# Optimization experiments

Hardware: AMD Instinct MI355X
Metric: run time of the kernel (lower is better)

## Reference

```python
import jax, jax.numpy as jnp
import numpy as np

B, NDEL, K, T = 32, 16, 10, 16384
N0 = int(round(T / 8))


def setup_inputs() -> dict:
    key = jax.random.key(0)
    k1, k2, k3 = jax.random.split(key, 3)
    shape = (B, NDEL, K)
    # stable complex-conjugate pole pairs: radius < 1 so the cascade decays
    r = jax.random.uniform(k1, shape, minval=0.5, maxval=0.99)
    theta = jax.random.uniform(k2, shape, minval=0.05, maxval=np.pi - 0.05)
    a1 = -2.0 * r * jnp.cos(theta)
    a2 = r * r
    b = jax.random.normal(k3, shape + (3,)) * 0.5
    # sos layout per biquad: (b0, b1, b2, a0, a1, a2), a0 = 1
    sos = jnp.concatenate(
        [b, jnp.ones(shape + (1,)), a1[..., None], a2[..., None]], axis=-1
    ).astype(jnp.float32)
    return {"output_biquad_cascade": sos}


def _sos_filter_impulse(sos):
    """Cascade-biquad IIR filter of a unit impulse.
    sos: [L, K, 6] -> output [L, T]. Transposed direct-form II, scan over time,
    vectorized over the L = B*Ndel independent filter lines."""
    L = sos.shape[0]
    a0 = sos[..., 3:4]
    bc = sos[..., 0:3] / a0  # [L, K, 3]
    ac = sos[..., 4:6] / a0  # [L, K, 2]
    # impulse input, time-major for scan: [T, L]
    x = jnp.zeros((T, L), dtype=sos.dtype).at[0, :].set(1.0)
    for k in range(K):  # fixed small cascade depth
        b0, b1, b2 = bc[:, k, 0], bc[:, k, 1], bc[:, k, 2]
        a1, a2 = ac[:, k, 0], ac[:, k, 1]

        def step(z, xt):
            z1, z2 = z
            y = b0 * xt + z1
            z1n = b1 * xt - a1 * y + z2
            z2n = b2 * xt - a2 * y
            return (z1n, z2n), y

        zero = jnp.zeros((L,), dtype=sos.dtype)
        _, x = jax.lax.scan(step, (zero, zero), x)  # x: [T, L]
    return x.T  # [L, T]


def reference(output_biquad_cascade):
    sos = output_biquad_cascade.reshape(B * NDEL, K, 6)
    y = _sos_filter_impulse(sos)  # [B*Ndel, T]
    # decay ratio: tail energy / head energy
    gamma = jnp.sum(jnp.abs(y[:, T - N0:]), axis=1) / jnp.sum(
        jnp.abs(y[:, :N0]), axis=1
    )
    gamma = gamma.reshape(B, NDEL)
    w = jnp.exp(gamma)
    loss = jnp.sum(gamma * w, axis=1) / jnp.sum(w, axis=1)  # softmax-weighted mean
    return jnp.sum(loss)
```

## Files before the change

### kernel.cpp

```cpp
#include <hip/hip_runtime.h>

#pragma clang fp contract(off)

#define B_    32
#define NDEL_ 16
#define K_    10
#define T_    16384
#define N0_   2048

__device__ __forceinline__ float dpp_shr1(float v) {
    int i = __builtin_bit_cast(int, v);
    int r = __builtin_amdgcn_update_dpp(0, i, 0x111 , 0xF, 0xF, true);
    return __builtin_bit_cast(float, r);
}

__global__ __launch_bounds__(256, 1)
void sos_gamma_kernel(const float* __restrict__ sos, float* __restrict__ out) {
#pragma clang fp contract(off)
    __builtin_amdgcn_s_setreg(6401, 0xC);

    const int tid  = threadIdx.x;
    const int wave = tid >> 6;
    const int lane = tid & 63;
    const int row  = lane >> 4;
    const int st   = lane & 15;
    const int d    = (wave << 2) | row;
    const int line = blockIdx.x * NDEL_ + d;

    float b0 = 0.f, b1 = 0.f, b2 = 0.f, a1 = 0.f, a2 = 0.f;
    if (st < K_) {
        const float* c = sos + (size_t)line * (K_ * 6) + st * 6;
        const float a0 = c[3];
        b0 = c[0] / a0;
        b1 = c[1] / a0;
        b2 = c[2] / a0;
        a1 = c[4] / a0;
        a2 = c[5] / a0;
    }

    float z1 = 0.f, z2 = 0.f;
    float hacc = 0.f, tacc = 0.f;

    float yA = 0.f, yB = 0.f;
    float xb1 = (st == 0) ? 1.0f : 0.0f;
    float xb2 = 0.f;

#define STEPX(XV, YOUT)                                \
    do {                                               \
        float x_ = (XV);                               \
        YOUT     = __builtin_fmaf(b0, x_, z1);         \
        float t3 = a1 * YOUT;                          \
        float t4 = __builtin_fmaf(b1, x_, -t3);        \
        float t6 = a2 * YOUT;                          \
        z1       = t4 + z2;                            \
        z2       = __builtin_fmaf(b2, x_, -t6);        \
    } while (0)

#define NOACC(YV)  do { } while (0)
#define HACC(YV)   do { hacc += fabsf(YV); } while (0)
#define TACC(YV)   do { tacc += fabsf(YV); } while (0)

#define TICK2(ACCUM)                                        \
    do {                                                    \
        float xA = xb1; xb2 = dpp_shr1(yA);                 \
        STEPX(xA, yB); ACCUM(yB);                           \
        float xB = xb2; xb1 = dpp_shr1(yB);                 \
        STEPX(xB, yA); ACCUM(yA);                           \
    } while (0)

#pragma unroll
    for (int p = 0; p < 9; ++p)    { TICK2(NOACC); }
#pragma unroll 4
    for (int p = 0; p < 1024; ++p) { TICK2(HACC); }
#pragma unroll 4
    for (int p = 0; p < 6144; ++p) { TICK2(NOACC); }
#pragma unroll 4
    for (int p = 0; p < 1024; ++p) { TICK2(TACC); }

#undef TICK2
#undef STEPX
#undef NOACC
#undef HACC
#undef TACC

    __shared__ float gam[NDEL_];
    if (st == 9) gam[d] = tacc / hacc;
    __syncthreads();

    if (tid == 0) {
        float num = 0.f, den = 0.f;
        for (int i = 0; i < NDEL_; ++i) {
            float g = gam[i];
            float w = expf(g);
            num += g * w;
            den += w;
        }
        atomicAdd(out, num / den);
    }
}

extern "C" void kernel_launch(void* const* d_in, const int* in_sizes, int n_in,
                              void* d_out, int out_size, void* d_ws, size_t ws_size,
                              hipStream_t stream) {
    (void)in_sizes; (void)n_in; (void)d_ws; (void)ws_size; (void)out_size;
    const float* sos = (const float*)d_in[0];
    float* out = (float*)d_out;

    hipMemsetAsync(out, 0, sizeof(float), stream);

    sos_gamma_kernel<<<B_, 256, 0, stream>>>(sos, out);
}
```

Baseline: 291.9 us.

## Split each batch across two blocks with a global atomic reduction

The grid doubles to 64 blocks. Each block handles 8 of the 16 delay lines of a batch, and each wave now runs only two filter lines (rows 0-1) instead of four. Per-line gamma values go to a workspace through atomics, and the second block to finish a batch does the softmax-weighted reduction. This spreads the work over more CUs, but adds an extra memset, global atomics and half-idle waves, while the serial recurrence length per lane stays the same.

Result: slower. 306.2 us (+4.9%).

```diff
diff --git a/kernel.cpp b/kernel.cpp
--- a/kernel.cpp
+++ b/kernel.cpp
@@ -15,7 +15,8 @@
 }
 
 __global__ __launch_bounds__(256, 1)
-void sos_gamma_kernel(const float* __restrict__ sos, float* __restrict__ out) {
+void sos_gamma_kernel(const float* __restrict__ sos, float* __restrict__ out,
+                      float* __restrict__ gws, int* __restrict__ cnt) {
 #pragma clang fp contract(off)
     __builtin_amdgcn_s_setreg(6401, 0xC);
 
@@ -24,26 +25,29 @@
     const int lane = tid & 63;
     const int row  = lane >> 4;
     const int st   = lane & 15;
-    const int d    = (wave << 2) | row;
-    const int line = blockIdx.x * NDEL_ + d;
+    const int g    = blockIdx.x;
+    const int b    = g >> 1;
+    const int d    = ((g & 1) << 3) | (wave << 1) | row;
+    const int line = b * NDEL_ + d;
 
-    float b0 = 0.f, b1 = 0.f, b2 = 0.f, a1 = 0.f, a2 = 0.f;
-    if (st < K_) {
-        const float* c = sos + (size_t)line * (K_ * 6) + st * 6;
-        const float a0 = c[3];
-        b0 = c[0] / a0;
-        b1 = c[1] / a0;
-        b2 = c[2] / a0;
-        a1 = c[4] / a0;
-        a2 = c[5] / a0;
-    }
+    if (row < 2) {
+        float b0 = 0.f, b1 = 0.f, b2 = 0.f, a1 = 0.f, a2 = 0.f;
+        if (st < K_) {
+            const float* c = sos + (size_t)line * (K_ * 6) + st * 6;
+            const float a0 = c[3];
+            b0 = c[0] / a0;
+            b1 = c[1] / a0;
+            b2 = c[2] / a0;
+            a1 = c[4] / a0;
+            a2 = c[5] / a0;
+        }
 
-    float z1 = 0.f, z2 = 0.f;
-    float hacc = 0.f, tacc = 0.f;
+        float z1 = 0.f, z2 = 0.f;
+        float hacc = 0.f, tacc = 0.f;
 
-    float yA = 0.f, yB = 0.f;
-    float xb1 = (st == 0) ? 1.0f : 0.0f;
-    float xb2 = 0.f;
+        float yA = 0.f, yB = 0.f;
+        float xb1 = (st == 0) ? 1.0f : 0.0f;
+        float xb2 = 0.f;
 
 #define STEPX(XV, YOUT)                                \
     do {                                               \
@@ -69,13 +73,13 @@
     } while (0)
 
 #pragma unroll
-    for (int p = 0; p < 9; ++p)    { TICK2(NOACC); }
+        for (int p = 0; p < 9; ++p)    { TICK2(NOACC); }
 #pragma unroll 4
-    for (int p = 0; p < 1024; ++p) { TICK2(HACC); }
+        for (int p = 0; p < 1024; ++p) { TICK2(HACC); }
 #pragma unroll 4
-    for (int p = 0; p < 6144; ++p) { TICK2(NOACC); }
+        for (int p = 0; p < 6144; ++p) { TICK2(NOACC); }
 #pragma unroll 4
-    for (int p = 0; p < 1024; ++p) { TICK2(TACC); }
+        for (int p = 0; p < 1024; ++p) { TICK2(TACC); }
 
 #undef TICK2
 #undef STEPX
@@ -83,30 +87,38 @@
 #undef HACC
 #undef TACC
 
-    __shared__ float gam[NDEL_];
-    if (st == 9) gam[d] = tacc / hacc;
+        if (st == 9) atomicAdd(&gws[b * NDEL_ + d], tacc / hacc);
+    }
+
     __syncthreads();
 
     if (tid == 0) {
-        float num = 0.f, den = 0.f;
-        for (int i = 0; i < NDEL_; ++i) {
-            float g = gam[i];
-            float w = expf(g);
-            num += g * w;
-            den += w;
+        __threadfence();
+        const int old = atomicAdd(&cnt[b], 1);
+        if (old == 1) {
+            float num = 0.f, den = 0.f;
+            for (int i = 0; i < NDEL_; ++i) {
+                float gg = atomicAdd(&gws[b * NDEL_ + i], 0.0f);
+                float w  = expf(gg);
+                num += gg * w;
+                den += w;
+            }
+            atomicAdd(out, num / den);
         }
-        atomicAdd(out, num / den);
     }
 }
 
 extern "C" void kernel_launch(void* const* d_in, const int* in_sizes, int n_in,
                               void* d_out, int out_size, void* d_ws, size_t ws_size,
                               hipStream_t stream) {
-    (void)in_sizes; (void)n_in; (void)d_ws; (void)ws_size; (void)out_size;
+    (void)in_sizes; (void)n_in; (void)ws_size; (void)out_size;
     const float* sos = (const float*)d_in[0];
     float* out = (float*)d_out;
+    float* gws = (float*)d_ws;
+    int*   cnt = (int*)(gws + B_ * NDEL_);
 
     hipMemsetAsync(out, 0, sizeof(float), stream);
+    hipMemsetAsync(d_ws, 0, B_ * NDEL_ * sizeof(float) + B_ * sizeof(int), stream);
 
-    sos_gamma_kernel<<<B_, 256, 0, stream>>>(sos, out);
+    sos_gamma_kernel<<<2 * B_, 256, 0, stream>>>(sos, out, gws, cnt);
 }
```
